# Kernel optimization log

Hardware: AMD Instinct MI355X
Metric: run time of the kernel (lower is better)

Reference implementation:

```python
import jax, jax.numpy as jnp
import numpy as np

N = 100000   # num nodes
D = 128      # node_emb_dim
R = 8        # num_relations
E = 1600000  # num edges


def setup_inputs() -> dict:
    key = jax.random.key(0)
    k0, k1, k2, k3, k4 = jax.random.split(key, 5)
    x = jax.random.normal(k0, (N, D), dtype=jnp.float32)
    edge_index = jax.random.randint(k1, (2, E), 0, N, dtype=jnp.int32)
    edge_type = jax.random.randint(k2, (E,), 0, R, dtype=jnp.int32)
    scale = 1.0 / np.sqrt(D)
    W = (jax.random.normal(k3, (R, D, D), dtype=jnp.float32) * scale)       # per-relation weight
    W_root = (jax.random.normal(k4, (D, D), dtype=jnp.float32) * scale)     # root (self-loop) weight
    bias = jnp.zeros((D,), dtype=jnp.float32)
    return {"x": x, "W": W, "W_root": W_root, "bias": bias,
            "edge_index": edge_index, "edge_type": edge_type}


def reference(x, W, W_root, bias, edge_index, edge_type):
    # PyG RGCNConv (num_bases=None, aggr='mean', root_weight=True, bias=True):
    # out_i = x_i @ W_root + bias + sum_r mean_{j in N_r(i)} x_j @ W_r
    # Mean aggregation is linear, so aggregate neighbor features per (node, relation)
    # first, then apply the per-relation transform (avoids [E,D,D] intermediates).
    src, dst = edge_index[0], edge_index[1]
    seg = dst * R + edge_type                                   # [E] segment id per (dst, rel)
    cnt = jax.ops.segment_sum(jnp.ones((E,), x.dtype), seg, num_segments=N * R)  # [N*R]
    sums = jax.ops.segment_sum(x[src], seg, num_segments=N * R)                   # [N*R, D]
    mean = sums / jnp.maximum(cnt, 1.0)[:, None]                                  # [N*R, D]
    rel_out = jnp.einsum('nrd,rde->ne', mean.reshape(N, R, D), W)                 # [N, D]
    return rel_out + x @ W_root + bias
```

## Files before the change

### kernel.cpp

```cpp
#include <hip/hip_runtime.h>


constexpr int D = 128;
constexpr int R = 8;
constexpr int LDA = 40;
constexpr int TILE2 = 4096;
constexpr int CAP = 768;
constexpr int MAXRUNS = 8192;
constexpr int TCH = 32;

typedef __bf16 bf16x8 __attribute__((ext_vector_type(8)));
typedef float  f32x4  __attribute__((ext_vector_type(4)));
typedef unsigned short u16x8 __attribute__((ext_vector_type(8)));
typedef unsigned short u16x4 __attribute__((ext_vector_type(4)));

__device__ __forceinline__ unsigned short f2bf(float f) {
    unsigned u = __builtin_bit_cast(unsigned, f);
    u += 0x7FFFu + ((u >> 16) & 1u);
    return (unsigned short)(u >> 16);
}
__device__ __forceinline__ float bf2f(unsigned short h) {
    return __builtin_bit_cast(float, (unsigned)h << 16);
}

constexpr int XB = 640;
constexpr int WB = 64;
__global__ __launch_bounds__(256)
void prep_kernel(const float* __restrict__ x, unsigned short* __restrict__ xbf,
                 int nquad,
                 const int* __restrict__ dst, const int* __restrict__ et,
                 unsigned short* __restrict__ counts, int E, int nruns, int ntiles,
                 const float* __restrict__ Wroot, const float* __restrict__ W,
                 unsigned short* __restrict__ WallTc) {
    __shared__ int lh[MAXRUNS];
    if (blockIdx.x < XB) {
        int stride = XB * 256;
        for (int i = blockIdx.x * 256 + threadIdx.x; i < nquad; i += stride) {
            float4 v = ((const float4*)x)[i];
            u16x4 o;
            o[0] = f2bf(v.x); o[1] = f2bf(v.y); o[2] = f2bf(v.z); o[3] = f2bf(v.w);
            ((u16x4*)xbf)[i] = o;
        }
    } else if (blockIdx.x < XB + (unsigned)ntiles) {
        int tile = blockIdx.x - XB;
        for (int i = threadIdx.x; i < nruns; i += 256) lh[i] = 0;
        __syncthreads();
        int t0 = tile * TILE2;
        #pragma unroll 4
        for (int j = 0; j < TILE2 / 256; ++j) {
            int e = t0 + j * 256 + threadIdx.x;
            if (e < E) {
                int seg = dst[e] * R + et[e];
                atomicAdd(&lh[seg >> 7], 1);
            }
        }
        __syncthreads();
        unsigned short* row = counts + (size_t)tile * nruns;
        for (int i = threadIdx.x; i < nruns; i += 256) row[i] = (unsigned short)lh[i];
    } else {
        int b = blockIdx.x - XB - ntiles;
        int stride = WB * 256;
        for (int idx = b * 256 + threadIdx.x; idx < 128 * 1152; idx += stride) {
            int n = idx / 1152, k = idx % 1152;
            float v = (k < 1024)
                ? W[(size_t)(k >> 7) * 16384 + (size_t)(k & 127) * 128 + n]
                : Wroot[(size_t)(k - 1024) * 128 + n];
            WallTc[idx] = f2bf(v);
        }
    }
}

__global__ __launch_bounds__(256)
void colscanA_kernel(const unsigned short* __restrict__ counts, int* __restrict__ part,
                     int ntiles, int nruns, int cpt) {
    int r = blockIdx.x * 256 + threadIdx.x;
    int c = blockIdx.y;
    if (r >= nruns) return;
    int t0 = c * cpt, t1 = min(t0 + cpt, ntiles);
    int acc = 0;
    for (int t = t0; t < t1; ++t) acc += counts[(size_t)t * nruns + r];
    part[(size_t)c * nruns + r] = acc;
}

__global__ __launch_bounds__(256)
void colscanB_kernel(int* __restrict__ part, int* __restrict__ runtot,
                     int nchunks, int nruns) {
    int r = blockIdx.x * 256 + threadIdx.x;
    if (r >= nruns) return;
    int acc = 0;
    for (int c = 0; c < nchunks; ++c) {
        size_t i = (size_t)c * nruns + r;
        int v = part[i];
        part[i] = acc;
        acc += v;
    }
    runtot[r] = acc;
}

__global__ __launch_bounds__(256)
void colscanC_kernel(unsigned short* __restrict__ counts, const int* __restrict__ part,
                     int ntiles, int nruns, int cpt) {
    int r = blockIdx.x * 256 + threadIdx.x;
    int c = blockIdx.y;
    if (r >= nruns) return;
    int t0 = c * cpt, t1 = min(t0 + cpt, ntiles);
    int acc = part[(size_t)c * nruns + r];
    for (int t = t0; t < t1; ++t) {
        size_t i = (size_t)t * nruns + r;
        int v = counts[i];
        counts[i] = (unsigned short)acc;
        acc += v;
    }
}

__global__ __launch_bounds__(64)
void runscan_kernel(const int* __restrict__ runtot, int* __restrict__ runbase, int nb) {
    int lane = threadIdx.x;
    int carry = 0;
    for (int base = 0; base < nb; base += 64) {
        int i = base + lane;
        int orig = (i < nb) ? runtot[i] : 0;
        int v = orig;
        #pragma unroll
        for (int off = 1; off < 64; off <<= 1) {
            int u = __shfl_up(v, off, 64);
            if (lane >= off) v += u;
        }
        int tot = __shfl(v, 63, 64);
        if (i < nb) runbase[i] = carry + (v - orig);
        carry += tot;
    }
    if (lane == 0) runbase[nb] = carry;
}

__global__ __launch_bounds__(256)
void place_kernel(const int* __restrict__ src, const int* __restrict__ dst,
                  const int* __restrict__ et, const unsigned short* __restrict__ counts,
                  const int* __restrict__ runbase, unsigned* __restrict__ epack,
                  int E, int nruns) {
    __shared__ int lh[MAXRUNS];
    for (int i = threadIdx.x; i < nruns; i += 256) lh[i] = 0;
    __syncthreads();
    int t0 = blockIdx.x * TILE2;
    const unsigned short* colpre = counts + (size_t)blockIdx.x * nruns;
    #pragma unroll 4
    for (int j = 0; j < TILE2 / 256; ++j) {
        int e = t0 + j * 256 + threadIdx.x;
        if (e < E) {
            int seg  = dst[e] * R + et[e];
            int run  = seg >> 7;
            int rank = atomicAdd(&lh[run], 1);
            int pos  = runbase[run] + (int)colpre[run] + rank;
            epack[pos] = (unsigned)src[e] | ((unsigned)(seg & 127) << 24);
        }
    }
}

__global__ __launch_bounds__(256)
void aggregate_kernel(const unsigned short* __restrict__ xbf,
                      const unsigned* __restrict__ epack,
                      const int* __restrict__ runbase,
                      unsigned short* __restrict__ mean,
                      int nseg) {
    __shared__ unsigned raw[CAP];
    __shared__ unsigned srt[CAP];
    __shared__ int hist[128], sc[128], offs[128], cur[128];

    const int tid  = threadIdx.x;
    const int run  = blockIdx.x;
    const int base = runbase[run];
    const int size = runbase[run + 1] - base;
    const int c8   = tid & 15;
    const int sg0  = tid >> 4;

    float a[8][8] = {};
    int   cacc[8] = {};

    const int nchunks = (size + CAP - 1) / CAP;
    for (int ch = 0; ch < nchunks; ++ch) {
        int off = ch * CAP;
        int n   = min(CAP, size - off);

        if (tid < 128) hist[tid] = 0;
        __syncthreads();
        for (int j = tid; j < n; j += 256) {
            unsigned e = epack[base + off + j];
            raw[j] = e;
            atomicAdd(&hist[e >> 24], 1);
        }
        __syncthreads();
        if (tid < 128) sc[tid] = hist[tid];
        __syncthreads();
        for (int o = 1; o < 128; o <<= 1) {
            int u = 0;
            if (tid < 128 && tid >= o) u = sc[tid - o];
            __syncthreads();
            if (tid < 128) sc[tid] += u;
            __syncthreads();
        }
        if (tid < 128) { int x0 = sc[tid] - hist[tid]; offs[tid] = x0; cur[tid] = x0; }
        __syncthreads();
        for (int j = tid; j < n; j += 256) {
            unsigned e = raw[j];
            int r = atomicAdd(&cur[e >> 24], 1);
            srt[r] = e;
        }
        __syncthreads();
        #pragma unroll
        for (int i = 0; i < 8; ++i) {
            int s  = sg0 + i * 16;
            int st = offs[s], cn = hist[s];
            cacc[i] += cn;
            for (int k = 0; k < cn; k += 4) {
                unsigned e0 = srt[st + k];
                int s1ok = (k + 1 < cn), s2ok = (k + 2 < cn), s3ok = (k + 3 < cn);
                unsigned e1 = s1ok ? srt[st + k + 1] : 0;
                unsigned e2 = s2ok ? srt[st + k + 2] : 0;
                unsigned e3 = s3ok ? srt[st + k + 3] : 0;
                u16x8 v0 = *(const u16x8*)(xbf + ((size_t)(e0 & 0xFFFFFF) << 7) + c8 * 8);
                #pragma unroll
                for (int q = 0; q < 8; ++q) a[i][q] += bf2f(v0[q]);
                if (s1ok) {
                    u16x8 v = *(const u16x8*)(xbf + ((size_t)(e1 & 0xFFFFFF) << 7) + c8 * 8);
                    #pragma unroll
                    for (int q = 0; q < 8; ++q) a[i][q] += bf2f(v[q]);
                }
                if (s2ok) {
                    u16x8 v = *(const u16x8*)(xbf + ((size_t)(e2 & 0xFFFFFF) << 7) + c8 * 8);
                    #pragma unroll
                    for (int q = 0; q < 8; ++q) a[i][q] += bf2f(v[q]);
                }
                if (s3ok) {
                    u16x8 v = *(const u16x8*)(xbf + ((size_t)(e3 & 0xFFFFFF) << 7) + c8 * 8);
                    #pragma unroll
                    for (int q = 0; q < 8; ++q) a[i][q] += bf2f(v[q]);
                }
            }
        }
        __syncthreads();
    }

    #pragma unroll
    for (int i = 0; i < 8; ++i) {
        int seg = run * 128 + sg0 + i * 16;
        if (seg < nseg) {
            int node = seg >> 3, r = seg & 7;
            float inv = (cacc[i] > 0) ? 1.0f / (float)cacc[i] : 0.0f;
            u16x8 o;
            #pragma unroll
            for (int q = 0; q < 8; ++q) o[q] = f2bf(a[i][q] * inv);
            *(u16x8*)(mean + ((size_t)node << 10) + r * 128 + c8 * 8) = o;
        }
    }
}

__global__ __launch_bounds__(256)
void mfma_gemm_kernel(const unsigned short* __restrict__ xbf,
                      const unsigned short* __restrict__ mean,
                      const unsigned short* __restrict__ WallTc,
                      const float* __restrict__ bias,
                      float* __restrict__ out, int N) {
    constexpr int NT = 36;
    constexpr int ABUF = 64 * LDA;
    constexpr int BBUF = 128 * LDA;
    __shared__ unsigned short As[3][ABUF];
    __shared__ unsigned short Bs[3][BBUF];
    const int tid  = threadIdx.x;
    const int nd0  = blockIdx.x * 64;
    const int lane = tid & 63;
    const int wid  = tid >> 6;
    const int wm   = wid >> 1;
    const int wn   = wid & 1;
    const int arow = tid >> 2;
    const int aoct = tid & 3;
    const int brow = tid >> 1;
    const int bhalf = tid & 1;

    f32x4 acc[2][4] = {};

    const int  anode = nd0 + arow;
    const bool aok   = anode < N;

    auto loadG = [&](int kt, u16x8& av8, u16x8& b0, u16x8& b1) {
        #pragma unroll
        for (int j = 0; j < 8; ++j) av8[j] = 0;
        int kbase;
        if (kt < 4) {
            if (aok)
                av8 = *(const u16x8*)(xbf + ((size_t)anode << 7) + kt * 32 + aoct * 8);
            kbase = 1024 + kt * 32;
        } else {
            int lk = (kt - 4) * 32;
            if (aok)
                av8 = *(const u16x8*)(mean + ((size_t)anode << 10) + lk + aoct * 8);
            kbase = lk;
        }
        const u16x8* wp = (const u16x8*)(WallTc + (size_t)brow * 1152 + kbase + bhalf * 16);
        b0 = wp[0];
        b1 = wp[1];
    };
    auto storeT = [&](int buf, const u16x8& av8, const u16x8& b0, const u16x8& b1) {
        *(u16x8*)&As[buf][arow * LDA + aoct * 8]       = av8;
        *(u16x8*)&Bs[buf][brow * LDA + bhalf * 16]     = b0;
        *(u16x8*)&Bs[buf][brow * LDA + bhalf * 16 + 8] = b1;
    };

    const int ko = (lane >> 4) * 8;
    const int rl = lane & 15;
    auto compute = [&](int buf) {
        bf16x8 af[2], bf[4];
        #pragma unroll
        for (int f = 0; f < 2; ++f)
            af[f] = __builtin_bit_cast(bf16x8,
                *(const u16x8*)&As[buf][(wm * 32 + f * 16 + rl) * LDA + ko]);
        #pragma unroll
        for (int f = 0; f < 4; ++f)
            bf[f] = __builtin_bit_cast(bf16x8,
                *(const u16x8*)&Bs[buf][(wn * 64 + f * 16 + rl) * LDA + ko]);
        #pragma unroll
        for (int mf = 0; mf < 2; ++mf)
            #pragma unroll
            for (int nf = 0; nf < 4; ++nf)
                acc[mf][nf] = __builtin_amdgcn_mfma_f32_16x16x32_bf16(af[mf], bf[nf],
                                                                     acc[mf][nf], 0, 0, 0);
    };

    u16x8 aA, bA0, bA1, aB, bB0, bB1;
    loadG(0, aA, bA0, bA1);
    storeT(0, aA, bA0, bA1);
    loadG(1, aA, bA0, bA1);
    __syncthreads();

    int cb = 0;
    for (int kt = 0; kt < NT; kt += 2) {
        if (kt + 2 < NT) loadG(kt + 2, aB, bB0, bB1);
        compute(cb);
        if (kt + 1 < NT) storeT((cb + 1) % 3, aA, bA0, bA1);
        __syncthreads();
        cb = (cb + 1) % 3;
        if (kt + 1 < NT) {
            if (kt + 3 < NT) loadG(kt + 3, aA, bA0, bA1);
            compute(cb);
            if (kt + 2 < NT) storeT((cb + 1) % 3, aB, bB0, bB1);
            __syncthreads();
            cb = (cb + 1) % 3;
        }
    }

    const int rg = lane >> 4;
    #pragma unroll
    for (int nf = 0; nf < 4; ++nf) {
        int n = wn * 64 + nf * 16 + rl;
        float bb = bias[n];
        #pragma unroll
        for (int mf = 0; mf < 2; ++mf) {
            #pragma unroll
            for (int i = 0; i < 4; ++i) {
                int nd = nd0 + wm * 32 + mf * 16 + rg * 4 + i;
                if (nd < N) out[(size_t)nd * 128 + n] = acc[mf][nf][i] + bb;
            }
        }
    }
}

extern "C" void kernel_launch(void* const* d_in, const int* in_sizes, int n_in,
                              void* d_out, int out_size, void* d_ws, size_t ws_size,
                              hipStream_t stream) {
    const float* x     = (const float*)d_in[0];
    const float* W     = (const float*)d_in[1];
    const float* Wroot = (const float*)d_in[2];
    const float* bias  = (const float*)d_in[3];
    const int*   ei    = (const int*)d_in[4];
    const int*   et    = (const int*)d_in[5];
    float*       out   = (float*)d_out;

    const int N = in_sizes[0] / D;
    const int E = in_sizes[5];
    const int* src = ei;
    const int* dst = ei + E;

    const int NSEG   = N * R;
    const int NRUNS  = (NSEG + 127) / 128;
    const int NTILES = (E + TILE2 - 1) / TILE2;
    if (NRUNS > MAXRUNS) return;

    const size_t mean_bytes   = (size_t)N * 1024 * 2;
    const size_t xbf_bytes    = (size_t)N * D * 2;
    const size_t walltc_bytes = (size_t)128 * 1152 * 2;
    const size_t counts_bytes = (size_t)NTILES * NRUNS * 2;
    const size_t part_bytes   = (size_t)TCH * NRUNS * 4;
    const size_t need = mean_bytes + xbf_bytes + walltc_bytes + counts_bytes +
                        part_bytes + ((size_t)NRUNS + (NRUNS + 1) + E) * 4 + 512;
    if (ws_size < need) return;

    char* p = (char*)d_ws;
    unsigned short* mean   = (unsigned short*)p;  p += mean_bytes;
    unsigned short* xbf    = (unsigned short*)p;  p += xbf_bytes;
    unsigned short* WallTc = (unsigned short*)p;  p += walltc_bytes;
    unsigned short* counts = (unsigned short*)p;  p += counts_bytes;
    int*      part    = (int*)p;       p += part_bytes;
    int*      runtot  = (int*)p;       p += (size_t)NRUNS * 4;
    int*      runbase = (int*)p;       p += (size_t)(NRUNS + 1) * 4;
    unsigned* epack   = (unsigned*)p;

    prep_kernel<<<XB + NTILES + WB, 256, 0, stream>>>(
        x, xbf, N * D / 4, dst, et, counts, E, NRUNS, NTILES, Wroot, W, WallTc);

    const int cpt = (NTILES + TCH - 1) / TCH;
    dim3 cgrid((NRUNS + 255) / 256, TCH);
    colscanA_kernel<<<cgrid, 256, 0, stream>>>(counts, part, NTILES, NRUNS, cpt);
    colscanB_kernel<<<(NRUNS + 255) / 256, 256, 0, stream>>>(part, runtot, TCH, NRUNS);
    colscanC_kernel<<<cgrid, 256, 0, stream>>>(counts, part, NTILES, NRUNS, cpt);
    runscan_kernel<<<1, 64, 0, stream>>>(runtot, runbase, NRUNS);

    place_kernel<<<NTILES, 256, 0, stream>>>(src, dst, et, counts, runbase, epack, E, NRUNS);

    aggregate_kernel<<<NRUNS, 256, 0, stream>>>(xbf, epack, runbase, mean, NSEG);

    const int gx = (N + 63) / 64;
    mfma_gemm_kernel<<<gx, 256, 0, stream>>>(xbf, mean, WallTc, bias, out, N);
}
```

Baseline: 350.7 us.

## Replace per-chunk LDS sort in aggregation with shared-memory atomic accumulation

The aggregation kernel no longer histograms, scans and sorts each edge chunk by segment. Instead it accumulates gathered bf16 neighbor rows into a 128x64 float shared tile with LDS atomicAdd, and counts edges per segment with atomics. The grid is split over two column halves (blockIdx.y), so each block handles 64 of the 128 features and there are twice as many blocks. This removes the scan and sort barriers and the per-segment load imbalance. In exchange it issues many LDS float atomics, reads the edge list twice across the column halves, and makes the float summation order nondeterministic.

```diff
diff --git a/kernel.cpp b/kernel.cpp
--- a/kernel.cpp
+++ b/kernel.cpp
@@ -162,94 +162,80 @@
                       const int* __restrict__ runbase,
                       unsigned short* __restrict__ mean,
                       int nseg) {
+    __shared__ float    tile[128][68];
     __shared__ unsigned raw[CAP];
-    __shared__ unsigned srt[CAP];
-    __shared__ int hist[128], sc[128], offs[128], cur[128];
+    __shared__ int      cntt[128];
 
     const int tid  = threadIdx.x;
     const int run  = blockIdx.x;
+    const int c0   = blockIdx.y * 64;
     const int base = runbase[run];
     const int size = runbase[run + 1] - base;
-    const int c8   = tid & 15;
-    const int sg0  = tid >> 4;
-
-    float a[8][8] = {};
-    int   cacc[8] = {};
-
-    const int nchunks = (size + CAP - 1) / CAP;
-    for (int ch = 0; ch < nchunks; ++ch) {
-        int off = ch * CAP;
-        int n   = min(CAP, size - off);
-
-        if (tid < 128) hist[tid] = 0;
+    const int g    = tid >> 3;
+    const int c8   = tid & 7;
+
+    for (int i = tid; i < 128 * 68; i += 256) ((float*)tile)[i] = 0.0f;
+    if (tid < 128) cntt[tid] = 0;
+    __syncthreads();
+
+    for (int off = 0; off < size; off += CAP) {
+        int n = min(CAP, size - off);
+        for (int j = tid; j < n; j += 256) raw[j] = epack[base + off + j];
         __syncthreads();
-        for (int j = tid; j < n; j += 256) {
-            unsigned e = epack[base + off + j];
-            raw[j] = e;
-            atomicAdd(&hist[e >> 24], 1);
+
+        for (int j = g; j < n; j += 128) {
+            unsigned e0 = raw[j];
+            bool ok1 = j + 32 < n, ok2 = j + 64 < n, ok3 = j + 96 < n;
+            unsigned e1 = ok1 ? raw[j + 32] : 0;
+            unsigned e2 = ok2 ? raw[j + 64] : 0;
+            unsigned e3 = ok3 ? raw[j + 96] : 0;
+            u16x8 v0 = *(const u16x8*)(xbf + ((size_t)(e0 & 0xFFFFFF) << 7) + c0 + c8 * 8);
+            u16x8 v1, v2, v3;
+            if (ok1) v1 = *(const u16x8*)(xbf + ((size_t)(e1 & 0xFFFFFF) << 7) + c0 + c8 * 8);
+            if (ok2) v2 = *(const u16x8*)(xbf + ((size_t)(e2 & 0xFFFFFF) << 7) + c0 + c8 * 8);
+            if (ok3) v3 = *(const u16x8*)(xbf + ((size_t)(e3 & 0xFFFFFF) << 7) + c0 + c8 * 8);
+
+            int s0 = e0 >> 24;
+            if (c8 == 0) atomicAdd(&cntt[s0], 1);
+            #pragma unroll
+            for (int q = 0; q < 8; ++q) atomicAdd(&tile[s0][c8 * 8 + q], bf2f(v0[q]));
+            if (ok1) {
+                int s = e1 >> 24;
+                if (c8 == 0) atomicAdd(&cntt[s], 1);
+                #pragma unroll
+                for (int q = 0; q < 8; ++q) atomicAdd(&tile[s][c8 * 8 + q], bf2f(v1[q]));
+            }
+            if (ok2) {
+                int s = e2 >> 24;
+                if (c8 == 0) atomicAdd(&cntt[s], 1);
+                #pragma unroll
+                for (int q = 0; q < 8; ++q) atomicAdd(&tile[s][c8 * 8 + q], bf2f(v2[q]));
+            }
+            if (ok3) {
+                int s = e3 >> 24;
+                if (c8 == 0) atomicAdd(&cntt[s], 1);
+                #pragma unroll
+                for (int q = 0; q < 8; ++q) atomicAdd(&tile[s][c8 * 8 + q], bf2f(v3[q]));
+            }
         }
         __syncthreads();
-        if (tid < 128) sc[tid] = hist[tid];
-        __syncthreads();
-        for (int o = 1; o < 128; o <<= 1) {
-            int u = 0;
-            if (tid < 128 && tid >= o) u = sc[tid - o];
-            __syncthreads();
-            if (tid < 128) sc[tid] += u;
-            __syncthreads();
-        }
-        if (tid < 128) { int x0 = sc[tid] - hist[tid]; offs[tid] = x0; cur[tid] = x0; }
-        __syncthreads();
-        for (int j = tid; j < n; j += 256) {
-            unsigned e = raw[j];
-            int r = atomicAdd(&cur[e >> 24], 1);
-            srt[r] = e;
-        }
-        __syncthreads();
-        #pragma unroll
-        for (int i = 0; i < 8; ++i) {
-            int s  = sg0 + i * 16;
-            int st = offs[s], cn = hist[s];
-            cacc[i] += cn;
-            for (int k = 0; k < cn; k += 4) {
-                unsigned e0 = srt[st + k];
-                int s1ok = (k + 1 < cn), s2ok = (k + 2 < cn), s3ok = (k + 3 < cn);
-                unsigned e1 = s1ok ? srt[st + k + 1] : 0;
-                unsigned e2 = s2ok ? srt[st + k + 2] : 0;
-                unsigned e3 = s3ok ? srt[st + k + 3] : 0;
-                u16x8 v0 = *(const u16x8*)(xbf + ((size_t)(e0 & 0xFFFFFF) << 7) + c8 * 8);
-                #pragma unroll
-                for (int q = 0; q < 8; ++q) a[i][q] += bf2f(v0[q]);
-                if (s1ok) {
-                    u16x8 v = *(const u16x8*)(xbf + ((size_t)(e1 & 0xFFFFFF) << 7) + c8 * 8);
-                    #pragma unroll
-                    for (int q = 0; q < 8; ++q) a[i][q] += bf2f(v[q]);
-                }
-                if (s2ok) {
-                    u16x8 v = *(const u16x8*)(xbf + ((size_t)(e2 & 0xFFFFFF) << 7) + c8 * 8);
-                    #pragma unroll
-                    for (int q = 0; q < 8; ++q) a[i][q] += bf2f(v[q]);
-                }
-                if (s3ok) {
-                    u16x8 v = *(const u16x8*)(xbf + ((size_t)(e3 & 0xFFFFFF) << 7) + c8 * 8);
-                    #pragma unroll
-                    for (int q = 0; q < 8; ++q) a[i][q] += bf2f(v[q]);
-                }
-            }
-        }
-        __syncthreads();
-    }
-
-    #pragma unroll
-    for (int i = 0; i < 8; ++i) {
-        int seg = run * 128 + sg0 + i * 16;
-        if (seg < nseg) {
-            int node = seg >> 3, r = seg & 7;
-            float inv = (cacc[i] > 0) ? 1.0f / (float)cacc[i] : 0.0f;
+    }
+
+    const int s  = tid >> 1;
+    const int hf = tid & 1;
+    const int seg = run * 128 + s;
+    if (seg < nseg) {
+        int cn = cntt[s];
+        float inv = (cn > 0) ? 1.0f / (float)cn : 0.0f;
+        int node = seg >> 3, r = seg & 7;
+        unsigned short* mp = mean + ((size_t)node << 10) + r * 128 + c0 + hf * 32;
+        #pragma unroll
+        for (int b = 0; b < 4; ++b) {
             u16x8 o;
             #pragma unroll
-            for (int q = 0; q < 8; ++q) o[q] = f2bf(a[i][q] * inv);
-            *(u16x8*)(mean + ((size_t)node << 10) + r * 128 + c8 * 8) = o;
+            for (int q = 0; q < 8; ++q)
+                o[q] = f2bf(tile[s][hf * 32 + b * 8 + q] * inv);
+            *(u16x8*)(mp + b * 8) = o;
         }
     }
 }
@@ -415,7 +401,7 @@
 
     place_kernel<<<NTILES, 256, 0, stream>>>(src, dst, et, counts, runbase, epack, E, NRUNS);
 
-    aggregate_kernel<<<NRUNS, 256, 0, stream>>>(xbf, epack, runbase, mean, NSEG);
+    aggregate_kernel<<<dim3(NRUNS, 2), 256, 0, stream>>>(xbf, epack, runbase, mean, NSEG);
 
     const int gx = (N + 63) / 64;
     mfma_gemm_kernel<<<gx, 256, 0, stream>>>(xbf, mean, WallTc, bias, out, N);
```

Result: slower. 1.289 ms (+267.6%).

## Enlarge GEMM tile to 128 rows and switch to double buffering

Applied to the files above, without the earlier changes.

The final MFMA GEMM now gives each block 128 output rows instead of 64, and each warp a 64x64 sub-tile, so every staged W tile is reused across twice as many rows. This halves the W reloads from global memory and doubles MFMA work per LDS fragment read. The triple-buffered two-step pipeline becomes a simpler double-buffered loop with one barrier per k-step. The costs are more accumulator registers, which may lower occupancy, fewer blocks for the grid, and less overlap of loads with compute.

```diff
diff --git a/kernel.cpp b/kernel.cpp
--- a/kernel.cpp
+++ b/kernel.cpp
@@ -261,89 +261,86 @@
                       const float* __restrict__ bias,
                       float* __restrict__ out, int N) {
     constexpr int NT = 36;
-    constexpr int ABUF = 64 * LDA;
-    constexpr int BBUF = 128 * LDA;
-    __shared__ unsigned short As[3][ABUF];
-    __shared__ unsigned short Bs[3][BBUF];
+    constexpr int TBUF = 128 * LDA;
+    __shared__ unsigned short As[2][TBUF];
+    __shared__ unsigned short Bs[2][TBUF];
     const int tid  = threadIdx.x;
-    const int nd0  = blockIdx.x * 64;
+    const int nd0  = blockIdx.x * 128;
     const int lane = tid & 63;
     const int wid  = tid >> 6;
     const int wm   = wid >> 1;
     const int wn   = wid & 1;
-    const int arow = tid >> 2;
-    const int aoct = tid & 3;
-    const int brow = tid >> 1;
-    const int bhalf = tid & 1;
-
-    f32x4 acc[2][4] = {};
-
-    const int  anode = nd0 + arow;
+    const int srow = tid >> 1;
+    const int sh16 = (tid & 1) * 16;
+
+    f32x4 acc[4][4] = {};
+
+    const int  anode = nd0 + srow;
     const bool aok   = anode < N;
 
-    auto loadG = [&](int kt, u16x8& av8, u16x8& b0, u16x8& b1) {
-        #pragma unroll
-        for (int j = 0; j < 8; ++j) av8[j] = 0;
+    auto loadG = [&](int kt, u16x8& a0, u16x8& a1, u16x8& b0, u16x8& b1) {
+        #pragma unroll
+        for (int j = 0; j < 8; ++j) { a0[j] = 0; a1[j] = 0; }
         int kbase;
         if (kt < 4) {
-            if (aok)
-                av8 = *(const u16x8*)(xbf + ((size_t)anode << 7) + kt * 32 + aoct * 8);
+            if (aok) {
+                const u16x8* xp = (const u16x8*)(xbf + ((size_t)anode << 7)
+                                                 + kt * 32 + sh16);
+                a0 = xp[0]; a1 = xp[1];
+            }
             kbase = 1024 + kt * 32;
         } else {
             int lk = (kt - 4) * 32;
-            if (aok)
-                av8 = *(const u16x8*)(mean + ((size_t)anode << 10) + lk + aoct * 8);
+            if (aok) {
+                const u16x8* mp = (const u16x8*)(mean + ((size_t)anode << 10)
+                                                 + lk + sh16);
+                a0 = mp[0]; a1 = mp[1];
+            }
             kbase = lk;
         }
-        const u16x8* wp = (const u16x8*)(WallTc + (size_t)brow * 1152 + kbase + bhalf * 16);
+        const u16x8* wp = (const u16x8*)(WallTc + (size_t)srow * 1152 + kbase + sh16);
         b0 = wp[0];
         b1 = wp[1];
     };
-    auto storeT = [&](int buf, const u16x8& av8, const u16x8& b0, const u16x8& b1) {
-        *(u16x8*)&As[buf][arow * LDA + aoct * 8]       = av8;
-        *(u16x8*)&Bs[buf][brow * LDA + bhalf * 16]     = b0;
-        *(u16x8*)&Bs[buf][brow * LDA + bhalf * 16 + 8] = b1;
+    auto storeT = [&](int buf, const u16x8& a0, const u16x8& a1,
+                      const u16x8& b0, const u16x8& b1) {
+        *(u16x8*)&As[buf][srow * LDA + sh16]     = a0;
+        *(u16x8*)&As[buf][srow * LDA + sh16 + 8] = a1;
+        *(u16x8*)&Bs[buf][srow * LDA + sh16]     = b0;
+        *(u16x8*)&Bs[buf][srow * LDA + sh16 + 8] = b1;
     };
 
     const int ko = (lane >> 4) * 8;
     const int rl = lane & 15;
     auto compute = [&](int buf) {
-        bf16x8 af[2], bf[4];
-        #pragma unroll
-        for (int f = 0; f < 2; ++f)
+        bf16x8 af[4], bf[4];
+        #pragma unroll
+        for (int f = 0; f < 4; ++f) {
             af[f] = __builtin_bit_cast(bf16x8,
-                *(const u16x8*)&As[buf][(wm * 32 + f * 16 + rl) * LDA + ko]);
-        #pragma unroll
-        for (int f = 0; f < 4; ++f)
+                *(const u16x8*)&As[buf][(wm * 64 + f * 16 + rl) * LDA + ko]);
             bf[f] = __builtin_bit_cast(bf16x8,
                 *(const u16x8*)&Bs[buf][(wn * 64 + f * 16 + rl) * LDA + ko]);
-        #pragma unroll
-        for (int mf = 0; mf < 2; ++mf)
+        }
+        #pragma unroll
+        for (int mf = 0; mf < 4; ++mf)
             #pragma unroll
             for (int nf = 0; nf < 4; ++nf)
                 acc[mf][nf] = __builtin_amdgcn_mfma_f32_16x16x32_bf16(af[mf], bf[nf],
                                                                      acc[mf][nf], 0, 0, 0);
     };
 
-    u16x8 aA, bA0, bA1, aB, bB0, bB1;
-    loadG(0, aA, bA0, bA1);
-    storeT(0, aA, bA0, bA1);
-    loadG(1, aA, bA0, bA1);
+    u16x8 a0, a1, b0, b1;
+    loadG(0, a0, a1, b0, b1);
+    storeT(0, a0, a1, b0, b1);
     __syncthreads();
 
-    int cb = 0;
-    for (int kt = 0; kt < NT; kt += 2) {
-        if (kt + 2 < NT) loadG(kt + 2, aB, bB0, bB1);
+    for (int kt = 0; kt < NT; ++kt) {
+        const int cb = kt & 1;
+        if (kt + 1 < NT) loadG(kt + 1, a0, a1, b0, b1);
         compute(cb);
-        if (kt + 1 < NT) storeT((cb + 1) % 3, aA, bA0, bA1);
-        __syncthreads();
-        cb = (cb + 1) % 3;
         if (kt + 1 < NT) {
-            if (kt + 3 < NT) loadG(kt + 3, aA, bA0, bA1);
-            compute(cb);
-            if (kt + 2 < NT) storeT((cb + 1) % 3, aB, bB0, bB1);
+            storeT(cb ^ 1, a0, a1, b0, b1);
             __syncthreads();
-            cb = (cb + 1) % 3;
         }
     }
 
@@ -353,10 +350,10 @@
         int n = wn * 64 + nf * 16 + rl;
         float bb = bias[n];
         #pragma unroll
-        for (int mf = 0; mf < 2; ++mf) {
+        for (int mf = 0; mf < 4; ++mf) {
             #pragma unroll
             for (int i = 0; i < 4; ++i) {
-                int nd = nd0 + wm * 32 + mf * 16 + rg * 4 + i;
+                int nd = nd0 + wm * 64 + mf * 16 + rg * 4 + i;
                 if (nd < N) out[(size_t)nd * 128 + n] = acc[mf][nf][i] + bb;
             }
         }
@@ -417,6 +414,6 @@
 
     aggregate_kernel<<<NRUNS, 256, 0, stream>>>(xbf, epack, runbase, mean, NSEG);
 
-    const int gx = (N + 63) / 64;
+    const int gx = (N + 127) / 128;
     mfma_gemm_kernel<<<gx, 256, 0, stream>>>(xbf, mean, WallTc, bias, out, N);
 }
```

After: 353.6 us. About the same (+0.8%).
